# Kernel tuning notes

Measured on AMD Instinct MI355X. Metric: run time of the kernel, lower is better.

## Reference

```python
import jax, jax.numpy as jnp
import numpy as np

B, T, S, H = 8, 256, 256, 512

def setup_inputs() -> dict:
    key = jax.random.key(0)
    k1, k2, k3, k4, k5, k6 = jax.random.split(key, 6)
    query = jax.random.normal(k1, (B, T, H), dtype=jnp.float32)
    encoder_outputs = jax.random.normal(k2, (B, S, H), dtype=jnp.float32)
    # lengths in [1, S] so every row has at least one valid source position
    src_lengths = jax.random.randint(k3, (B,), 1, S + 1, dtype=jnp.int64)
    scale = 1.0 / np.sqrt(H)
    W_h = jax.random.normal(k4, (H, H), dtype=jnp.float32) * scale  # nn.Linear weight (out, in)
    W_s = jax.random.normal(k5, (H, H), dtype=jnp.float32) * scale
    v = jax.random.normal(k6, (H,), dtype=jnp.float32) * scale     # nn.Linear(H,1) weight squeezed
    return {"query": query, "encoder_outputs": encoder_outputs,
            "src_lengths": src_lengths, "W_h": W_h, "W_s": W_s, "v": v}

def reference(query, encoder_outputs, src_lengths, W_h, W_s, v):
    # Linear without bias: y = x @ W^T
    enc_f = jnp.einsum('bsh,oh->bso', encoder_outputs, W_h)   # (B,S,H)
    qry_f = jnp.einsum('bth,oh->bto', query, W_s)             # (B,T,H)
    # additive score: v^T tanh(enc_f + qry_f), broadcast over (T,S)
    scores = jnp.einsum('btsh,h->bts',
                        jnp.tanh(enc_f[:, None, :, :] + qry_f[:, :, None, :]), v)  # (B,T,S)
    mask = jnp.arange(S)[None, :] >= src_lengths[:, None]      # (B,S) True = pad
    scores = jnp.where(mask[:, None, :], -jnp.inf, scores)
    attn_weights = jax.nn.softmax(scores, axis=-1)             # (B,T,S)
    attn_out = jnp.einsum('bts,bsh->bth', attn_weights, encoder_outputs)
    return attn_out
```

## Files before the change

kernel.cpp:

```cpp
#include <hip/hip_runtime.h>
#include <hip/hip_cooperative_groups.h>
#include <cstddef>
#include <math.h>

namespace cg = cooperative_groups;

#define BD 8
#define TD 256
#define SD 256
#define HD 512
#define K2F 2.885390081777927f

#define EXP2(x) __builtin_amdgcn_exp2f(x)
#define RCP(x)  __builtin_amdgcn_rcpf(x)

typedef __attribute__((ext_vector_type(8))) _Float16 half8;
typedef __attribute__((ext_vector_type(4))) _Float16 half4;
typedef __attribute__((ext_vector_type(4))) float float4v;

__device__ __forceinline__ float exp2_sat(float x) {
    return EXP2(fminf(fmaxf(x, -80.0f), 80.0f));
}

#define LSTR 40

__global__ __launch_bounds__(512) void fused_kernel(
    const float* __restrict__ enc,
    const float* __restrict__ qry,
    const float* __restrict__ Wh,
    const float* __restrict__ Ws,
    const float* __restrict__ v,
    const int*   __restrict__ lens,
    float* __restrict__ encT,
    float* __restrict__ qryf,
    float* __restrict__ out)
{
    __shared__ float smem[7168];

    const int bid = blockIdx.x;
    const int tid = threadIdx.x;
    const int l   = tid & 63;
    const int w   = tid >> 6;
    const int rf  = l & 15;
    const int q   = l >> 4;

    {
        _Float16* LA = (_Float16*)smem;
        _Float16* LB = (_Float16*)(smem + 1280);

        const int x  = bid & 7;
        const int k  = bid >> 3;
        const bool isq = k >= 32;
        const int kk = k & 31;
        const int my = (isq ? 32 : 0) + x * 4 + (kk & 3);
        const int n0 = (kk >> 2) * 64;
        const int m0 = my * 64;

        const int srow = tid >> 3;
        const int scol = (tid & 7) * 4;
        const float* Abase = isq
            ? qry + (size_t)(m0 - 2048 + srow) * HD + scol
            : enc + (size_t)(m0 + srow) * HD + scol;
        const float* Bbase = (isq ? Ws : Wh) + (size_t)(n0 + srow) * HD + scol;

        const int mi = (w & 3) * 16;
        const int ni = (w >> 2) * 32;

        float4v acc[2] = {{0,0,0,0},{0,0,0,0}};

        float4 a0 = *(const float4*)(Abase);
        float4 b0 = *(const float4*)(Bbase);

        for (int ks = 0; ks < 16; ++ks) {
            if (ks) __syncthreads();
            {
                half4 ha, hb;
                ha[0]=(_Float16)a0.x; ha[1]=(_Float16)a0.y; ha[2]=(_Float16)a0.z; ha[3]=(_Float16)a0.w;
                hb[0]=(_Float16)b0.x; hb[1]=(_Float16)b0.y; hb[2]=(_Float16)b0.z; hb[3]=(_Float16)b0.w;
                *(half4*)&LA[srow * LSTR + scol] = ha;
                *(half4*)&LB[srow * LSTR + scol] = hb;
            }
            __syncthreads();
            if (ks + 1 < 16) {
                const int ko = (ks + 1) * 32;
                a0 = *(const float4*)(Abase + ko);
                b0 = *(const float4*)(Bbase + ko);
            }
            half8 ah = *(const half8*)&LA[(mi + rf) * LSTR + q * 8];
            #pragma unroll
            for (int j = 0; j < 2; ++j) {
                half8 bh = *(const half8*)&LB[(ni + j * 16 + rf) * LSTR + q * 8];
                acc[j] = __builtin_amdgcn_mfma_f32_16x16x32_f16(ah, bh, acc[j], 0, 0, 0);
            }
        }

        if (!isq) {
            const int b  = m0 >> 8;
            const int sb = (m0 & 255) + mi + q * 4;
            float* base = encT + (size_t)b * HD * SD;
            #pragma unroll
            for (int j = 0; j < 2; ++j) {
                float4 o = make_float4(exp2_sat(acc[j][0]*K2F), exp2_sat(acc[j][1]*K2F),
                                       exp2_sat(acc[j][2]*K2F), exp2_sat(acc[j][3]*K2F));
                *(float4*)(base + (size_t)(n0 + ni + j * 16 + rf) * SD + sb) = o;
            }
        } else {
            const int mrow = (m0 - 2048) + mi + q * 4;
            #pragma unroll
            for (int j = 0; j < 2; ++j)
                #pragma unroll
                for (int r = 0; r < 4; ++r)
                    qryf[(size_t)(mrow + r) * HD + n0 + ni + j * 16 + rf] =
                        exp2_sat(acc[j][r] * K2F);
        }
    }

    cg::this_grid().sync();

    {
        float* qls = smem;
        float* pls = smem + 2048;
        float* wls = smem + 6144;

        const int b  = bid & 7;
        const int t0 = (bid >> 3) * 4;

        {
            const float* qf = qryf + ((size_t)b * TD + t0) * HD;
            float4 qv;
            qv.x = qf[0 * HD + tid]; qv.y = qf[1 * HD + tid];
            qv.z = qf[2 * HD + tid]; qv.w = qf[3 * HD + tid];
            *(float4*)&qls[tid * 4] = qv;
        }
        __syncthreads();

        float a[4][4];
        #pragma unroll
        for (int t = 0; t < 4; ++t)
            #pragma unroll
            for (int c = 0; c < 4; ++c) a[t][c] = 0.0f;
        {
            const float* ep = encT + (size_t)b * HD * SD + (size_t)(w * 64) * SD + l * 4;
            const int jbase = w * 64;
            #pragma unroll 4
            for (int jj = 0; jj < 64; ++jj) {
                float4 e = *(const float4*)(ep + (size_t)jj * SD);
                float4 q4 = *(const float4*)&qls[(jbase + jj) * 4];
                float vj = v[jbase + jj];
                float ev[4] = {e.x, e.y, e.z, e.w};
                float qv[4] = {q4.x, q4.y, q4.z, q4.w};
                #pragma unroll
                for (int t = 0; t < 4; ++t)
                    #pragma unroll
                    for (int c = 0; c < 4; ++c) {
                        float p = fmaf(ev[c], qv[t], 1.0f);
                        a[t][c] = fmaf(vj, RCP(p), a[t][c]);
                    }
            }
        }
        if (w < 4) {
            #pragma unroll
            for (int t = 0; t < 4; ++t)
                *(float4*)&pls[(w * 4 + t) * 256 + l * 4] =
                    make_float4(a[t][0], a[t][1], a[t][2], a[t][3]);
        }
        __syncthreads();
        if (w >= 4) {
            #pragma unroll
            for (int t = 0; t < 4; ++t) {
                float4 c4 = *(const float4*)&pls[((w - 4) * 4 + t) * 256 + l * 4];
                c4.x += a[t][0]; c4.y += a[t][1]; c4.z += a[t][2]; c4.w += a[t][3];
                *(float4*)&pls[((w - 4) * 4 + t) * 256 + l * 4] = c4;
            }
        }
        __syncthreads();

        if (w < 4) {
            const int t = w;
            float p[4] = {0, 0, 0, 0};
            #pragma unroll
            for (int g = 0; g < 4; ++g) {
                float4 pp = *(const float4*)&pls[(g * 4 + t) * 256 + l * 4];
                p[0] += pp.x; p[1] += pp.y; p[2] += pp.z; p[3] += pp.w;
            }
            const int len = lens[b];
            const int s0 = l * 4;
            float sc[4];
            #pragma unroll
            for (int c = 0; c < 4; ++c)
                sc[c] = (s0 + c < len) ? -2.0f * p[c] : -INFINITY;
            float mx = fmaxf(fmaxf(sc[0], sc[1]), fmaxf(sc[2], sc[3]));
            #pragma unroll
            for (int off = 32; off; off >>= 1) mx = fmaxf(mx, __shfl_xor(mx, off));
            float ex[4]; float sum = 0.0f;
            #pragma unroll
            for (int c = 0; c < 4; ++c) { ex[c] = __expf(sc[c] - mx); sum += ex[c]; }
            #pragma unroll
            for (int off = 32; off; off >>= 1) sum += __shfl_xor(sum, off);
            const float inv = RCP(sum);
            *(float4*)&wls[t * SD + s0] = make_float4(ex[0]*inv, ex[1]*inv, ex[2]*inv, ex[3]*inv);
        }
        __syncthreads();

        const int sg = tid >> 7;
        const int h4 = (tid & 127) * 4;
        float* avred = pls;
        float4 o[4] = {{0,0,0,0},{0,0,0,0},{0,0,0,0},{0,0,0,0}};
        {
            const float* eb = enc + (size_t)b * SD * HD + h4;
            #pragma unroll 2
            for (int ss = 0; ss < 64; ++ss) {
                const int s = sg * 64 + ss;
                float4 evv = *(const float4*)(eb + (size_t)s * HD);
                float wt[4];
                #pragma unroll
                for (int t = 0; t < 4; ++t) wt[t] = wls[t * SD + s];
                #pragma unroll
                for (int t = 0; t < 4; ++t) {
                    o[t].x = fmaf(wt[t], evv.x, o[t].x);
                    o[t].y = fmaf(wt[t], evv.y, o[t].y);
                    o[t].z = fmaf(wt[t], evv.z, o[t].z);
                    o[t].w = fmaf(wt[t], evv.w, o[t].w);
                }
            }
        }
        if (sg < 2) {
            #pragma unroll
            for (int t = 0; t < 4; ++t)
                *(float4*)&avred[(size_t)(sg * 4 + t) * 512 + h4] = o[t];
        }
        __syncthreads();
        if (sg >= 2) {
            #pragma unroll
            for (int t = 0; t < 4; ++t) {
                float4 c4 = *(const float4*)&avred[(size_t)((sg - 2) * 4 + t) * 512 + h4];
                c4.x += o[t].x; c4.y += o[t].y; c4.z += o[t].z; c4.w += o[t].w;
                *(float4*)&avred[(size_t)((sg - 2) * 4 + t) * 512 + h4] = c4;
            }
        }
        __syncthreads();

        {
            const int t  = tid >> 7;
            const int hh = (tid & 127) * 4;
            float4 x0 = *(const float4*)&avred[(size_t)(0 * 4 + t) * 512 + hh];
            float4 x1 = *(const float4*)&avred[(size_t)(1 * 4 + t) * 512 + hh];
            float4 r = make_float4(x0.x + x1.x, x0.y + x1.y, x0.z + x1.z, x0.w + x1.w);
            *(float4*)(out + ((size_t)b * TD + t0 + t) * HD + hh) = r;
        }
    }
}

__global__ __launch_bounds__(256) void proj_fb(
    const float* __restrict__ enc, const float* __restrict__ qry,
    const float* __restrict__ Wh,  const float* __restrict__ Ws,
    float* __restrict__ encT, float* __restrict__ qryf)
{
    __shared__ _Float16 LA[64 * LSTR], LB[64 * LSTR];

    const int tid = threadIdx.x;
    const int l = tid & 63, w = tid >> 6;
    const int rf = l & 15, q = l >> 4;
    const int my = blockIdx.y;
    const bool isq = my >= 32;
    const int m0 = my * 64;
    const int n0 = blockIdx.x * 64;

    const int srow = tid >> 2;
    const int scol = (tid & 3) * 8;
    const float* Abase = isq
        ? qry + (size_t)(m0 - 2048 + srow) * HD + scol
        : enc + (size_t)(m0 + srow) * HD + scol;
    const float* Bbase = (isq ? Ws : Wh) + (size_t)(n0 + srow) * HD + scol;

    const int mi = (w & 1) * 32, ni = (w >> 1) * 32;
    float4v acc[2][2] = {{{0,0,0,0},{0,0,0,0}},{{0,0,0,0},{0,0,0,0}}};

    float4 a0 = *(const float4*)(Abase);
    float4 a1 = *(const float4*)(Abase + 4);
    float4 b0 = *(const float4*)(Bbase);
    float4 b1 = *(const float4*)(Bbase + 4);

    for (int ks = 0; ks < 16; ++ks) {
        if (ks) __syncthreads();
        {
            float af[8] = {a0.x,a0.y,a0.z,a0.w,a1.x,a1.y,a1.z,a1.w};
            float bf[8] = {b0.x,b0.y,b0.z,b0.w,b1.x,b1.y,b1.z,b1.w};
            half8 ha, hb;
            #pragma unroll
            for (int i = 0; i < 8; ++i) { ha[i] = (_Float16)af[i]; hb[i] = (_Float16)bf[i]; }
            *(half8*)&LA[srow * LSTR + scol] = ha;
            *(half8*)&LB[srow * LSTR + scol] = hb;
        }
        __syncthreads();
        if (ks + 1 < 16) {
            const int ko = (ks + 1) * 32;
            a0 = *(const float4*)(Abase + ko);
            a1 = *(const float4*)(Abase + ko + 4);
            b0 = *(const float4*)(Bbase + ko);
            b1 = *(const float4*)(Bbase + ko + 4);
        }
        half8 ah[2], bh[2];
        #pragma unroll
        for (int i = 0; i < 2; ++i) {
            ah[i] = *(const half8*)&LA[(mi + i * 16 + rf) * LSTR + q * 8];
            bh[i] = *(const half8*)&LB[(ni + i * 16 + rf) * LSTR + q * 8];
        }
        #pragma unroll
        for (int i = 0; i < 2; ++i)
            #pragma unroll
            for (int j = 0; j < 2; ++j)
                acc[i][j] = __builtin_amdgcn_mfma_f32_16x16x32_f16(ah[i], bh[j], acc[i][j], 0, 0, 0);
    }

    if (!isq) {
        const int b  = m0 >> 8;
        const int sb = (m0 & 255) + mi + q * 4;
        float* base = encT + (size_t)b * HD * SD;
        #pragma unroll
        for (int i = 0; i < 2; ++i)
            #pragma unroll
            for (int j = 0; j < 2; ++j) {
                float4 o = make_float4(exp2_sat(acc[i][j][0]*K2F), exp2_sat(acc[i][j][1]*K2F),
                                       exp2_sat(acc[i][j][2]*K2F), exp2_sat(acc[i][j][3]*K2F));
                *(float4*)(base + (size_t)(n0 + ni + j * 16 + rf) * SD + sb + i * 16) = o;
            }
    } else {
        const int mrow = (m0 - 2048) + mi + q * 4;
        #pragma unroll
        for (int i = 0; i < 2; ++i)
            #pragma unroll
            for (int j = 0; j < 2; ++j)
                #pragma unroll
                for (int r = 0; r < 4; ++r)
                    qryf[(size_t)(mrow + i * 16 + r) * HD + n0 + ni + j * 16 + rf] =
                        exp2_sat(acc[i][j][r] * K2F);
    }
}

__global__ __launch_bounds__(512) void attn_fb(
    const float* __restrict__ enc, const float* __restrict__ encT,
    const float* __restrict__ qryf, const float* __restrict__ v,
    const int* __restrict__ lens, float* __restrict__ out)
{
    __shared__ float qls[HD * 4];
    __shared__ float pls[8 * 4 * 256];
    __shared__ float wls[4 * SD];

    const int blk = blockIdx.x;
    const int b   = blk >> 6;
    const int t0  = (blk & 63) * 4;
    const int tid = threadIdx.x;
    const int w   = tid >> 6;
    const int l   = tid & 63;

    {
        const float* qf = qryf + ((size_t)b * TD + t0) * HD;
        float4 qv;
        qv.x = qf[0 * HD + tid]; qv.y = qf[1 * HD + tid];
        qv.z = qf[2 * HD + tid]; qv.w = qf[3 * HD + tid];
        *(float4*)&qls[tid * 4] = qv;
    }
    __syncthreads();

    float a[4][4];
    #pragma unroll
    for (int t = 0; t < 4; ++t)
        #pragma unroll
        for (int c = 0; c < 4; ++c) a[t][c] = 0.0f;
    {
        const float* ep = encT + (size_t)b * HD * SD + (size_t)(w * 64) * SD + l * 4;
        const int jbase = w * 64;
        #pragma unroll 4
        for (int jj = 0; jj < 64; ++jj) {
            float4 e = *(const float4*)(ep + (size_t)jj * SD);
            float4 q4 = *(const float4*)&qls[(jbase + jj) * 4];
            float vj = v[jbase + jj];
            float ev[4] = {e.x, e.y, e.z, e.w};
            float qv[4] = {q4.x, q4.y, q4.z, q4.w};
            #pragma unroll
            for (int t = 0; t < 4; ++t)
                #pragma unroll
                for (int c = 0; c < 4; ++c) {
                    float p = fmaf(ev[c], qv[t], 1.0f);
                    a[t][c] = fmaf(vj, RCP(p), a[t][c]);
                }
        }
    }
    #pragma unroll
    for (int t = 0; t < 4; ++t)
        *(float4*)&pls[(w * 4 + t) * 256 + l * 4] = make_float4(a[t][0], a[t][1], a[t][2], a[t][3]);
    __syncthreads();

    if (w < 4) {
        const int t = w;
        float p[4] = {0, 0, 0, 0};
        #pragma unroll
        for (int g = 0; g < 8; ++g) {
            float4 pp = *(const float4*)&pls[(g * 4 + t) * 256 + l * 4];
            p[0] += pp.x; p[1] += pp.y; p[2] += pp.z; p[3] += pp.w;
        }
        const int len = lens[b];
        const int s0 = l * 4;
        float sc[4];
        #pragma unroll
        for (int c = 0; c < 4; ++c)
            sc[c] = (s0 + c < len) ? -2.0f * p[c] : -INFINITY;
        float mx = fmaxf(fmaxf(sc[0], sc[1]), fmaxf(sc[2], sc[3]));
        #pragma unroll
        for (int off = 32; off; off >>= 1) mx = fmaxf(mx, __shfl_xor(mx, off));
        float ex[4]; float sum = 0.0f;
        #pragma unroll
        for (int c = 0; c < 4; ++c) { ex[c] = __expf(sc[c] - mx); sum += ex[c]; }
        #pragma unroll
        for (int off = 32; off; off >>= 1) sum += __shfl_xor(sum, off);
        const float inv = RCP(sum);
        *(float4*)&wls[t * SD + s0] = make_float4(ex[0]*inv, ex[1]*inv, ex[2]*inv, ex[3]*inv);
    }
    __syncthreads();

    const int g  = tid >> 7;
    const int h4 = (tid & 127) * 4;
    float* avred = pls;
    {
        const float* eb = enc + (size_t)b * SD * HD + h4;
        float4 o[4] = {{0,0,0,0},{0,0,0,0},{0,0,0,0},{0,0,0,0}};
        #pragma unroll 2
        for (int ss = 0; ss < 64; ++ss) {
            const int s = g * 64 + ss;
            float4 evv = *(const float4*)(eb + (size_t)s * HD);
            float wt[4];
            #pragma unroll
            for (int t = 0; t < 4; ++t) wt[t] = wls[t * SD + s];
            #pragma unroll
            for (int t = 0; t < 4; ++t) {
                o[t].x = fmaf(wt[t], evv.x, o[t].x);
                o[t].y = fmaf(wt[t], evv.y, o[t].y);
                o[t].z = fmaf(wt[t], evv.z, o[t].z);
                o[t].w = fmaf(wt[t], evv.w, o[t].w);
            }
        }
        #pragma unroll
        for (int t = 0; t < 4; ++t)
            *(float4*)&avred[(size_t)(g * 4 + t) * 512 + h4] = o[t];
    }
    __syncthreads();
    {
        const int t  = tid >> 7;
        const int hh = (tid & 127) * 4;
        float4 r = {0, 0, 0, 0};
        #pragma unroll
        for (int gg = 0; gg < 4; ++gg) {
            float4 x = *(const float4*)&avred[(size_t)(gg * 4 + t) * 512 + hh];
            r.x += x.x; r.y += x.y; r.z += x.z; r.w += x.w;
        }
        *(float4*)(out + ((size_t)b * TD + t0 + t) * HD + hh) = r;
    }
}

extern "C" void kernel_launch(void* const* d_in, const int* in_sizes, int n_in,
                              void* d_out, int out_size, void* d_ws, size_t ws_size,
                              hipStream_t stream) {
    const float* query = (const float*)d_in[0];
    const float* enc   = (const float*)d_in[1];
    const int*   lens  = (const int*)d_in[2];
    const float* W_h   = (const float*)d_in[3];
    const float* W_s   = (const float*)d_in[4];
    const float* v     = (const float*)d_in[5];
    float* out = (float*)d_out;

    char* ws = (char*)d_ws;
    float* encT = (float*)(ws);
    float* qryf = (float*)(ws + ((size_t)4 << 20));

    int nb = 0;
    hipError_t oerr = hipOccupancyMaxActiveBlocksPerMultiprocessor(
        &nb, (const void*)fused_kernel, 512, 0);
    bool coop_ok = (oerr == hipSuccess) && (nb * 256 >= 512);

    if (coop_ok) {
        void* args[] = {
            (void*)&enc, (void*)&query, (void*)&W_h, (void*)&W_s,
            (void*)&v, (void*)&lens, (void*)&encT, (void*)&qryf, (void*)&out
        };
        hipError_t lerr = hipLaunchCooperativeKernel((const void*)fused_kernel,
                                                     dim3(512), dim3(512), args, 0, stream);
        if (lerr == hipSuccess) return;
    }

    dim3 pgrid(HD / 64, 64);
    proj_fb<<<pgrid, 256, 0, stream>>>(enc, query, W_h, W_s, encT, qryf);
    attn_fb<<<BD * (TD / 4), 512, 0, stream>>>(enc, encT, qryf, v, lens, out);
}
```

Measured before the change: 121.0 us.

## Split attention phase across 1024 cooperative blocks with two timesteps each

```diff
diff --git a/kernel.cpp b/kernel.cpp
--- a/kernel.cpp
+++ b/kernel.cpp
@@ -24,231 +24,254 @@
 
 #define LSTR 40
 
-__global__ __launch_bounds__(512) void fused_kernel(
-    const float* __restrict__ enc,
-    const float* __restrict__ qry,
-    const float* __restrict__ Wh,
-    const float* __restrict__ Ws,
-    const float* __restrict__ v,
-    const int*   __restrict__ lens,
-    float* __restrict__ encT,
-    float* __restrict__ qryf,
-    float* __restrict__ out)
+__device__ __forceinline__ void phaseA(
+    int bid, int tid, float* smem,
+    const float* __restrict__ enc, const float* __restrict__ qry,
+    const float* __restrict__ Wh,  const float* __restrict__ Ws,
+    float* __restrict__ encT, float* __restrict__ qryf)
+{
+    const int l  = tid & 63;
+    const int w  = tid >> 6;
+    const int rf = l & 15;
+    const int q  = l >> 4;
+
+    _Float16* LA = (_Float16*)smem;
+    _Float16* LB = (_Float16*)(smem + 1280);
+
+    const int x  = bid & 7;
+    const int k  = bid >> 3;
+    const bool isq = k >= 32;
+    const int kk = k & 31;
+    const int my = (isq ? 32 : 0) + x * 4 + (kk & 3);
+    const int n0 = (kk >> 2) * 64;
+    const int m0 = my * 64;
+
+    const int srow = tid >> 3;
+    const int scol = (tid & 7) * 4;
+    const float* Abase = isq
+        ? qry + (size_t)(m0 - 2048 + srow) * HD + scol
+        : enc + (size_t)(m0 + srow) * HD + scol;
+    const float* Bbase = (isq ? Ws : Wh) + (size_t)(n0 + srow) * HD + scol;
+
+    const int mi = (w & 3) * 16;
+    const int ni = (w >> 2) * 32;
+
+    float4v acc[2] = {{0,0,0,0},{0,0,0,0}};
+
+    float4 a0 = *(const float4*)(Abase);
+    float4 b0 = *(const float4*)(Bbase);
+
+    for (int ks = 0; ks < 16; ++ks) {
+        if (ks) __syncthreads();
+        {
+            half4 ha, hb;
+            ha[0]=(_Float16)a0.x; ha[1]=(_Float16)a0.y; ha[2]=(_Float16)a0.z; ha[3]=(_Float16)a0.w;
+            hb[0]=(_Float16)b0.x; hb[1]=(_Float16)b0.y; hb[2]=(_Float16)b0.z; hb[3]=(_Float16)b0.w;
+            *(half4*)&LA[srow * LSTR + scol] = ha;
+            *(half4*)&LB[srow * LSTR + scol] = hb;
+        }
+        __syncthreads();
+        if (ks + 1 < 16) {
+            const int ko = (ks + 1) * 32;
+            a0 = *(const float4*)(Abase + ko);
+            b0 = *(const float4*)(Bbase + ko);
+        }
+        half8 ah = *(const half8*)&LA[(mi + rf) * LSTR + q * 8];
+        #pragma unroll
+        for (int j = 0; j < 2; ++j) {
+            half8 bh = *(const half8*)&LB[(ni + j * 16 + rf) * LSTR + q * 8];
+            acc[j] = __builtin_amdgcn_mfma_f32_16x16x32_f16(ah, bh, acc[j], 0, 0, 0);
+        }
+    }
+
+    if (!isq) {
+        const int b  = m0 >> 8;
+        const int sb = (m0 & 255) + mi + q * 4;
+        float* base = encT + (size_t)b * HD * SD;
+        #pragma unroll
+        for (int j = 0; j < 2; ++j) {
+            float4 o = make_float4(exp2_sat(acc[j][0]*K2F), exp2_sat(acc[j][1]*K2F),
+                                   exp2_sat(acc[j][2]*K2F), exp2_sat(acc[j][3]*K2F));
+            *(float4*)(base + (size_t)(n0 + ni + j * 16 + rf) * SD + sb) = o;
+        }
+    } else {
+        const int mrow = (m0 - 2048) + mi + q * 4;
+        #pragma unroll
+        for (int j = 0; j < 2; ++j)
+            #pragma unroll
+            for (int r = 0; r < 4; ++r)
+                qryf[(size_t)(mrow + r) * HD + n0 + ni + j * 16 + rf] =
+                    exp2_sat(acc[j][r] * K2F);
+    }
+}
+
+template<int TT>
+__device__ __forceinline__ void phaseB(
+    int b, int t0, int tid, float* smem,
+    const float* __restrict__ enc, const float* __restrict__ encT,
+    const float* __restrict__ qryf, const float* __restrict__ v,
+    const int* __restrict__ lens, float* __restrict__ out)
+{
+    const int l = tid & 63;
+    const int w = tid >> 6;
+
+    float* qls = smem;
+    float* pls = smem + 512 * TT;
+    float* wls = smem + 1536 * TT;
+
+    {
+        const float* qf = qryf + ((size_t)b * TD + t0) * HD;
+        #pragma unroll
+        for (int t = 0; t < TT; ++t) qls[tid * TT + t] = qf[t * HD + tid];
+    }
+    __syncthreads();
+
+    float a[TT][4];
+    #pragma unroll
+    for (int t = 0; t < TT; ++t)
+        #pragma unroll
+        for (int c = 0; c < 4; ++c) a[t][c] = 0.0f;
+    {
+        const float* ep = encT + (size_t)b * HD * SD + (size_t)(w * 64) * SD + l * 4;
+        const int jbase = w * 64;
+        #pragma unroll 4
+        for (int jj = 0; jj < 64; ++jj) {
+            float4 e = *(const float4*)(ep + (size_t)jj * SD);
+            float vj = v[jbase + jj];
+            float qv[TT];
+            #pragma unroll
+            for (int t = 0; t < TT; ++t) qv[t] = qls[(jbase + jj) * TT + t];
+            float ev[4] = {e.x, e.y, e.z, e.w};
+            #pragma unroll
+            for (int t = 0; t < TT; ++t)
+                #pragma unroll
+                for (int c = 0; c < 4; ++c) {
+                    float p = fmaf(ev[c], qv[t], 1.0f);
+                    a[t][c] = fmaf(vj, RCP(p), a[t][c]);
+                }
+        }
+    }
+    if (w < 4) {
+        #pragma unroll
+        for (int t = 0; t < TT; ++t)
+            *(float4*)&pls[(w * TT + t) * 256 + l * 4] =
+                make_float4(a[t][0], a[t][1], a[t][2], a[t][3]);
+    }
+    __syncthreads();
+    if (w >= 4) {
+        #pragma unroll
+        for (int t = 0; t < TT; ++t) {
+            float4 c4 = *(const float4*)&pls[((w - 4) * TT + t) * 256 + l * 4];
+            c4.x += a[t][0]; c4.y += a[t][1]; c4.z += a[t][2]; c4.w += a[t][3];
+            *(float4*)&pls[((w - 4) * TT + t) * 256 + l * 4] = c4;
+        }
+    }
+    __syncthreads();
+
+    if (w < TT) {
+        const int t = w;
+        float p[4] = {0, 0, 0, 0};
+        #pragma unroll
+        for (int g = 0; g < 4; ++g) {
+            float4 pp = *(const float4*)&pls[(g * TT + t) * 256 + l * 4];
+            p[0] += pp.x; p[1] += pp.y; p[2] += pp.z; p[3] += pp.w;
+        }
+        const int len = lens[b];
+        const int s0 = l * 4;
+        float sc[4];
+        #pragma unroll
+        for (int c = 0; c < 4; ++c)
+            sc[c] = (s0 + c < len) ? -2.0f * p[c] : -INFINITY;
+        float mx = fmaxf(fmaxf(sc[0], sc[1]), fmaxf(sc[2], sc[3]));
+        #pragma unroll
+        for (int off = 32; off; off >>= 1) mx = fmaxf(mx, __shfl_xor(mx, off));
+        float ex[4]; float sum = 0.0f;
+        #pragma unroll
+        for (int c = 0; c < 4; ++c) { ex[c] = __expf(sc[c] - mx); sum += ex[c]; }
+        #pragma unroll
+        for (int off = 32; off; off >>= 1) sum += __shfl_xor(sum, off);
+        const float inv = RCP(sum);
+        *(float4*)&wls[t * SD + s0] = make_float4(ex[0]*inv, ex[1]*inv, ex[2]*inv, ex[3]*inv);
+    }
+    __syncthreads();
+
+    const int sg = tid >> 7;
+    const int h4 = (tid & 127) * 4;
+    float* avred = pls;
+    float4 o[TT];
+    #pragma unroll
+    for (int t = 0; t < TT; ++t) o[t] = make_float4(0.f, 0.f, 0.f, 0.f);
+    {
+        const float* eb = enc + (size_t)b * SD * HD + h4;
+        #pragma unroll 2
+        for (int ss = 0; ss < 64; ++ss) {
+            const int s = sg * 64 + ss;
+            float4 evv = *(const float4*)(eb + (size_t)s * HD);
+            float wt[TT];
+            #pragma unroll
+            for (int t = 0; t < TT; ++t) wt[t] = wls[t * SD + s];
+            #pragma unroll
+            for (int t = 0; t < TT; ++t) {
+                o[t].x = fmaf(wt[t], evv.x, o[t].x);
+                o[t].y = fmaf(wt[t], evv.y, o[t].y);
+                o[t].z = fmaf(wt[t], evv.z, o[t].z);
+                o[t].w = fmaf(wt[t], evv.w, o[t].w);
+            }
+        }
+    }
+    if (sg < 2) {
+        #pragma unroll
+        for (int t = 0; t < TT; ++t)
+            *(float4*)&avred[(size_t)(sg * TT + t) * 512 + h4] = o[t];
+    }
+    __syncthreads();
+    if (sg >= 2) {
+        #pragma unroll
+        for (int t = 0; t < TT; ++t) {
+            float4 c4 = *(const float4*)&avred[(size_t)((sg - 2) * TT + t) * 512 + h4];
+            c4.x += o[t].x; c4.y += o[t].y; c4.z += o[t].z; c4.w += o[t].w;
+            *(float4*)&avred[(size_t)((sg - 2) * TT + t) * 512 + h4] = c4;
+        }
+    }
+    __syncthreads();
+
+    if (tid < TT * 128) {
+        const int t  = tid >> 7;
+        const int hh = (tid & 127) * 4;
+        float4 x0 = *(const float4*)&avred[(size_t)(0 * TT + t) * 512 + hh];
+        float4 x1 = *(const float4*)&avred[(size_t)(1 * TT + t) * 512 + hh];
+        float4 r = make_float4(x0.x + x1.x, x0.y + x1.y, x0.z + x1.z, x0.w + x1.w);
+        *(float4*)(out + ((size_t)b * TD + t0 + t) * HD + hh) = r;
+    }
+}
+
+__global__ __launch_bounds__(512) void fused1024(
+    const float* __restrict__ enc, const float* __restrict__ qry,
+    const float* __restrict__ Wh,  const float* __restrict__ Ws,
+    const float* __restrict__ v,   const int* __restrict__ lens,
+    float* __restrict__ encT, float* __restrict__ qryf, float* __restrict__ out)
+{
+    __shared__ float smem[3584];
+    const int bid = blockIdx.x;
+    if (bid < 512)
+        phaseA(bid, threadIdx.x, smem, enc, qry, Wh, Ws, encT, qryf);
+    cg::this_grid().sync();
+    phaseB<2>(bid & 7, (bid >> 3) * 2, threadIdx.x, smem,
+              enc, encT, qryf, v, lens, out);
+}
+
+__global__ __launch_bounds__(512) void fused512(
+    const float* __restrict__ enc, const float* __restrict__ qry,
+    const float* __restrict__ Wh,  const float* __restrict__ Ws,
+    const float* __restrict__ v,   const int* __restrict__ lens,
+    float* __restrict__ encT, float* __restrict__ qryf, float* __restrict__ out)
 {
     __shared__ float smem[7168];
-
     const int bid = blockIdx.x;
-    const int tid = threadIdx.x;
-    const int l   = tid & 63;
-    const int w   = tid >> 6;
-    const int rf  = l & 15;
-    const int q   = l >> 4;
-
-    {
-        _Float16* LA = (_Float16*)smem;
-        _Float16* LB = (_Float16*)(smem + 1280);
-
-        const int x  = bid & 7;
-        const int k  = bid >> 3;
-        const bool isq = k >= 32;
-        const int kk = k & 31;
-        const int my = (isq ? 32 : 0) + x * 4 + (kk & 3);
-        const int n0 = (kk >> 2) * 64;
-        const int m0 = my * 64;
-
-        const int srow = tid >> 3;
-        const int scol = (tid & 7) * 4;
-        const float* Abase = isq
-            ? qry + (size_t)(m0 - 2048 + srow) * HD + scol
-            : enc + (size_t)(m0 + srow) * HD + scol;
-        const float* Bbase = (isq ? Ws : Wh) + (size_t)(n0 + srow) * HD + scol;
-
-        const int mi = (w & 3) * 16;
-        const int ni = (w >> 2) * 32;
-
-        float4v acc[2] = {{0,0,0,0},{0,0,0,0}};
-
-        float4 a0 = *(const float4*)(Abase);
-        float4 b0 = *(const float4*)(Bbase);
-
-        for (int ks = 0; ks < 16; ++ks) {
-            if (ks) __syncthreads();
-            {
-                half4 ha, hb;
-                ha[0]=(_Float16)a0.x; ha[1]=(_Float16)a0.y; ha[2]=(_Float16)a0.z; ha[3]=(_Float16)a0.w;
-                hb[0]=(_Float16)b0.x; hb[1]=(_Float16)b0.y; hb[2]=(_Float16)b0.z; hb[3]=(_Float16)b0.w;
-                *(half4*)&LA[srow * LSTR + scol] = ha;
-                *(half4*)&LB[srow * LSTR + scol] = hb;
-            }
-            __syncthreads();
-            if (ks + 1 < 16) {
-                const int ko = (ks + 1) * 32;
-                a0 = *(const float4*)(Abase + ko);
-                b0 = *(const float4*)(Bbase + ko);
-            }
-            half8 ah = *(const half8*)&LA[(mi + rf) * LSTR + q * 8];
-            #pragma unroll
-            for (int j = 0; j < 2; ++j) {
-                half8 bh = *(const half8*)&LB[(ni + j * 16 + rf) * LSTR + q * 8];
-                acc[j] = __builtin_amdgcn_mfma_f32_16x16x32_f16(ah, bh, acc[j], 0, 0, 0);
-            }
-        }
-
-        if (!isq) {
-            const int b  = m0 >> 8;
-            const int sb = (m0 & 255) + mi + q * 4;
-            float* base = encT + (size_t)b * HD * SD;
-            #pragma unroll
-            for (int j = 0; j < 2; ++j) {
-                float4 o = make_float4(exp2_sat(acc[j][0]*K2F), exp2_sat(acc[j][1]*K2F),
-                                       exp2_sat(acc[j][2]*K2F), exp2_sat(acc[j][3]*K2F));
-                *(float4*)(base + (size_t)(n0 + ni + j * 16 + rf) * SD + sb) = o;
-            }
-        } else {
-            const int mrow = (m0 - 2048) + mi + q * 4;
-            #pragma unroll
-            for (int j = 0; j < 2; ++j)
-                #pragma unroll
-                for (int r = 0; r < 4; ++r)
-                    qryf[(size_t)(mrow + r) * HD + n0 + ni + j * 16 + rf] =
-                        exp2_sat(acc[j][r] * K2F);
-        }
-    }
-
+    phaseA(bid, threadIdx.x, smem, enc, qry, Wh, Ws, encT, qryf);
     cg::this_grid().sync();
-
-    {
-        float* qls = smem;
-        float* pls = smem + 2048;
-        float* wls = smem + 6144;
-
-        const int b  = bid & 7;
-        const int t0 = (bid >> 3) * 4;
-
-        {
-            const float* qf = qryf + ((size_t)b * TD + t0) * HD;
-            float4 qv;
-            qv.x = qf[0 * HD + tid]; qv.y = qf[1 * HD + tid];
-            qv.z = qf[2 * HD + tid]; qv.w = qf[3 * HD + tid];
-            *(float4*)&qls[tid * 4] = qv;
-        }
-        __syncthreads();
-
-        float a[4][4];
-        #pragma unroll
-        for (int t = 0; t < 4; ++t)
-            #pragma unroll
-            for (int c = 0; c < 4; ++c) a[t][c] = 0.0f;
-        {
-            const float* ep = encT + (size_t)b * HD * SD + (size_t)(w * 64) * SD + l * 4;
-            const int jbase = w * 64;
-            #pragma unroll 4
-            for (int jj = 0; jj < 64; ++jj) {
-                float4 e = *(const float4*)(ep + (size_t)jj * SD);
-                float4 q4 = *(const float4*)&qls[(jbase + jj) * 4];
-                float vj = v[jbase + jj];
-                float ev[4] = {e.x, e.y, e.z, e.w};
-                float qv[4] = {q4.x, q4.y, q4.z, q4.w};
-                #pragma unroll
-                for (int t = 0; t < 4; ++t)
-                    #pragma unroll
-                    for (int c = 0; c < 4; ++c) {
-                        float p = fmaf(ev[c], qv[t], 1.0f);
-                        a[t][c] = fmaf(vj, RCP(p), a[t][c]);
-                    }
-            }
-        }
-        if (w < 4) {
-            #pragma unroll
-            for (int t = 0; t < 4; ++t)
-                *(float4*)&pls[(w * 4 + t) * 256 + l * 4] =
-                    make_float4(a[t][0], a[t][1], a[t][2], a[t][3]);
-        }
-        __syncthreads();
-        if (w >= 4) {
-            #pragma unroll
-            for (int t = 0; t < 4; ++t) {
-                float4 c4 = *(const float4*)&pls[((w - 4) * 4 + t) * 256 + l * 4];
-                c4.x += a[t][0]; c4.y += a[t][1]; c4.z += a[t][2]; c4.w += a[t][3];
-                *(float4*)&pls[((w - 4) * 4 + t) * 256 + l * 4] = c4;
-            }
-        }
-        __syncthreads();
-
-        if (w < 4) {
-            const int t = w;
-            float p[4] = {0, 0, 0, 0};
-            #pragma unroll
-            for (int g = 0; g < 4; ++g) {
-                float4 pp = *(const float4*)&pls[(g * 4 + t) * 256 + l * 4];
-                p[0] += pp.x; p[1] += pp.y; p[2] += pp.z; p[3] += pp.w;
-            }
-            const int len = lens[b];
-            const int s0 = l * 4;
-            float sc[4];
-            #pragma unroll
-            for (int c = 0; c < 4; ++c)
-                sc[c] = (s0 + c < len) ? -2.0f * p[c] : -INFINITY;
-            float mx = fmaxf(fmaxf(sc[0], sc[1]), fmaxf(sc[2], sc[3]));
-            #pragma unroll
-            for (int off = 32; off; off >>= 1) mx = fmaxf(mx, __shfl_xor(mx, off));
-            float ex[4]; float sum = 0.0f;
-            #pragma unroll
-            for (int c = 0; c < 4; ++c) { ex[c] = __expf(sc[c] - mx); sum += ex[c]; }
-            #pragma unroll
-            for (int off = 32; off; off >>= 1) sum += __shfl_xor(sum, off);
-            const float inv = RCP(sum);
-            *(float4*)&wls[t * SD + s0] = make_float4(ex[0]*inv, ex[1]*inv, ex[2]*inv, ex[3]*inv);
-        }
-        __syncthreads();
-
-        const int sg = tid >> 7;
-        const int h4 = (tid & 127) * 4;
-        float* avred = pls;
-        float4 o[4] = {{0,0,0,0},{0,0,0,0},{0,0,0,0},{0,0,0,0}};
-        {
-            const float* eb = enc + (size_t)b * SD * HD + h4;
-            #pragma unroll 2
-            for (int ss = 0; ss < 64; ++ss) {
-                const int s = sg * 64 + ss;
-                float4 evv = *(const float4*)(eb + (size_t)s * HD);
-                float wt[4];
-                #pragma unroll
-                for (int t = 0; t < 4; ++t) wt[t] = wls[t * SD + s];
-                #pragma unroll
-                for (int t = 0; t < 4; ++t) {
-                    o[t].x = fmaf(wt[t], evv.x, o[t].x);
-                    o[t].y = fmaf(wt[t], evv.y, o[t].y);
-                    o[t].z = fmaf(wt[t], evv.z, o[t].z);
-                    o[t].w = fmaf(wt[t], evv.w, o[t].w);
-                }
-            }
-        }
-        if (sg < 2) {
-            #pragma unroll
-            for (int t = 0; t < 4; ++t)
-                *(float4*)&avred[(size_t)(sg * 4 + t) * 512 + h4] = o[t];
-        }
-        __syncthreads();
-        if (sg >= 2) {
-            #pragma unroll
-            for (int t = 0; t < 4; ++t) {
-                float4 c4 = *(const float4*)&avred[(size_t)((sg - 2) * 4 + t) * 512 + h4];
-                c4.x += o[t].x; c4.y += o[t].y; c4.z += o[t].z; c4.w += o[t].w;
-                *(float4*)&avred[(size_t)((sg - 2) * 4 + t) * 512 + h4] = c4;
-            }
-        }
-        __syncthreads();
-
-        {
-            const int t  = tid >> 7;
-            const int hh = (tid & 127) * 4;
-            float4 x0 = *(const float4*)&avred[(size_t)(0 * 4 + t) * 512 + hh];
-            float4 x1 = *(const float4*)&avred[(size_t)(1 * 4 + t) * 512 + hh];
-            float4 r = make_float4(x0.x + x1.x, x0.y + x1.y, x0.z + x1.z, x0.w + x1.w);
-            *(float4*)(out + ((size_t)b * TD + t0 + t) * HD + hh) = r;
-        }
-    }
+    phaseB<4>(bid & 7, (bid >> 3) * 4, threadIdx.x, smem,
+              enc, encT, qryf, v, lens, out);
 }
 
 __global__ __launch_bounds__(256) void proj_fb(
@@ -473,17 +496,25 @@
     float* encT = (float*)(ws);
     float* qryf = (float*)(ws + ((size_t)4 << 20));
 
+    void* args[] = {
+        (void*)&enc, (void*)&query, (void*)&W_h, (void*)&W_s,
+        (void*)&v, (void*)&lens, (void*)&encT, (void*)&qryf, (void*)&out
+    };
+
     int nb = 0;
     hipError_t oerr = hipOccupancyMaxActiveBlocksPerMultiprocessor(
-        &nb, (const void*)fused_kernel, 512, 0);
-    bool coop_ok = (oerr == hipSuccess) && (nb * 256 >= 512);
-
-    if (coop_ok) {
-        void* args[] = {
-            (void*)&enc, (void*)&query, (void*)&W_h, (void*)&W_s,
-            (void*)&v, (void*)&lens, (void*)&encT, (void*)&qryf, (void*)&out
-        };
-        hipError_t lerr = hipLaunchCooperativeKernel((const void*)fused_kernel,
+        &nb, (const void*)fused1024, 512, 0);
+    if (oerr == hipSuccess && nb >= 4) {
+        hipError_t lerr = hipLaunchCooperativeKernel((const void*)fused1024,
+                                                     dim3(1024), dim3(512), args, 0, stream);
+        if (lerr == hipSuccess) return;
+    }
+
+    nb = 0;
+    oerr = hipOccupancyMaxActiveBlocksPerMultiprocessor(
+        &nb, (const void*)fused512, 512, 0);
+    if (oerr == hipSuccess && nb >= 2) {
+        hipError_t lerr = hipLaunchCooperativeKernel((const void*)fused512,
                                                      dim3(512), dim3(512), args, 0, stream);
         if (lerr == hipSuccess) return;
     }
```

Result: no change. 120.8 us (-0.1%).

## Replace cooperative fused kernel with two 1024-thread kernels and 8-row attention tiles

Applied to the files above, without the earlier changes.

```diff
diff --git a/kernel.cpp b/kernel.cpp
--- a/kernel.cpp
+++ b/kernel.cpp
@@ -1,9 +1,6 @@
 #include <hip/hip_runtime.h>
-#include <hip/hip_cooperative_groups.h>
 #include <cstddef>
 #include <math.h>
-
-namespace cg = cooperative_groups;
 
 #define BD 8
 #define TD 256
@@ -24,362 +21,121 @@
 
 #define LSTR 40
 
-__global__ __launch_bounds__(512) void fused_kernel(
-    const float* __restrict__ enc,
-    const float* __restrict__ qry,
-    const float* __restrict__ Wh,
-    const float* __restrict__ Ws,
-    const float* __restrict__ v,
-    const int*   __restrict__ lens,
-    float* __restrict__ encT,
-    float* __restrict__ qryf,
-    float* __restrict__ out)
-{
-    __shared__ float smem[7168];
-
-    const int bid = blockIdx.x;
-    const int tid = threadIdx.x;
-    const int l   = tid & 63;
-    const int w   = tid >> 6;
-    const int rf  = l & 15;
-    const int q   = l >> 4;
-
-    {
-        _Float16* LA = (_Float16*)smem;
-        _Float16* LB = (_Float16*)(smem + 1280);
-
-        const int x  = bid & 7;
-        const int k  = bid >> 3;
-        const bool isq = k >= 32;
-        const int kk = k & 31;
-        const int my = (isq ? 32 : 0) + x * 4 + (kk & 3);
-        const int n0 = (kk >> 2) * 64;
-        const int m0 = my * 64;
-
-        const int srow = tid >> 3;
-        const int scol = (tid & 7) * 4;
-        const float* Abase = isq
-            ? qry + (size_t)(m0 - 2048 + srow) * HD + scol
-            : enc + (size_t)(m0 + srow) * HD + scol;
-        const float* Bbase = (isq ? Ws : Wh) + (size_t)(n0 + srow) * HD + scol;
-
-        const int mi = (w & 3) * 16;
-        const int ni = (w >> 2) * 32;
-
-        float4v acc[2] = {{0,0,0,0},{0,0,0,0}};
-
-        float4 a0 = *(const float4*)(Abase);
-        float4 b0 = *(const float4*)(Bbase);
-
-        for (int ks = 0; ks < 16; ++ks) {
-            if (ks) __syncthreads();
-            {
-                half4 ha, hb;
-                ha[0]=(_Float16)a0.x; ha[1]=(_Float16)a0.y; ha[2]=(_Float16)a0.z; ha[3]=(_Float16)a0.w;
-                hb[0]=(_Float16)b0.x; hb[1]=(_Float16)b0.y; hb[2]=(_Float16)b0.z; hb[3]=(_Float16)b0.w;
-                *(half4*)&LA[srow * LSTR + scol] = ha;
-                *(half4*)&LB[srow * LSTR + scol] = hb;
-            }
-            __syncthreads();
-            if (ks + 1 < 16) {
-                const int ko = (ks + 1) * 32;
-                a0 = *(const float4*)(Abase + ko);
-                b0 = *(const float4*)(Bbase + ko);
-            }
-            half8 ah = *(const half8*)&LA[(mi + rf) * LSTR + q * 8];
-            #pragma unroll
-            for (int j = 0; j < 2; ++j) {
-                half8 bh = *(const half8*)&LB[(ni + j * 16 + rf) * LSTR + q * 8];
-                acc[j] = __builtin_amdgcn_mfma_f32_16x16x32_f16(ah, bh, acc[j], 0, 0, 0);
-            }
-        }
-
-        if (!isq) {
-            const int b  = m0 >> 8;
-            const int sb = (m0 & 255) + mi + q * 4;
-            float* base = encT + (size_t)b * HD * SD;
-            #pragma unroll
-            for (int j = 0; j < 2; ++j) {
-                float4 o = make_float4(exp2_sat(acc[j][0]*K2F), exp2_sat(acc[j][1]*K2F),
-                                       exp2_sat(acc[j][2]*K2F), exp2_sat(acc[j][3]*K2F));
-                *(float4*)(base + (size_t)(n0 + ni + j * 16 + rf) * SD + sb) = o;
-            }
-        } else {
-            const int mrow = (m0 - 2048) + mi + q * 4;
-            #pragma unroll
-            for (int j = 0; j < 2; ++j)
-                #pragma unroll
-                for (int r = 0; r < 4; ++r)
-                    qryf[(size_t)(mrow + r) * HD + n0 + ni + j * 16 + rf] =
-                        exp2_sat(acc[j][r] * K2F);
-        }
-    }
-
-    cg::this_grid().sync();
-
-    {
-        float* qls = smem;
-        float* pls = smem + 2048;
-        float* wls = smem + 6144;
-
-        const int b  = bid & 7;
-        const int t0 = (bid >> 3) * 4;
-
-        {
-            const float* qf = qryf + ((size_t)b * TD + t0) * HD;
-            float4 qv;
-            qv.x = qf[0 * HD + tid]; qv.y = qf[1 * HD + tid];
-            qv.z = qf[2 * HD + tid]; qv.w = qf[3 * HD + tid];
-            *(float4*)&qls[tid * 4] = qv;
-        }
-        __syncthreads();
-
-        float a[4][4];
-        #pragma unroll
-        for (int t = 0; t < 4; ++t)
-            #pragma unroll
-            for (int c = 0; c < 4; ++c) a[t][c] = 0.0f;
-        {
-            const float* ep = encT + (size_t)b * HD * SD + (size_t)(w * 64) * SD + l * 4;
-            const int jbase = w * 64;
-            #pragma unroll 4
-            for (int jj = 0; jj < 64; ++jj) {
-                float4 e = *(const float4*)(ep + (size_t)jj * SD);
-                float4 q4 = *(const float4*)&qls[(jbase + jj) * 4];
-                float vj = v[jbase + jj];
-                float ev[4] = {e.x, e.y, e.z, e.w};
-                float qv[4] = {q4.x, q4.y, q4.z, q4.w};
-                #pragma unroll
-                for (int t = 0; t < 4; ++t)
-                    #pragma unroll
-                    for (int c = 0; c < 4; ++c) {
-                        float p = fmaf(ev[c], qv[t], 1.0f);
-                        a[t][c] = fmaf(vj, RCP(p), a[t][c]);
-                    }
-            }
-        }
-        if (w < 4) {
-            #pragma unroll
-            for (int t = 0; t < 4; ++t)
-                *(float4*)&pls[(w * 4 + t) * 256 + l * 4] =
-                    make_float4(a[t][0], a[t][1], a[t][2], a[t][3]);
-        }
-        __syncthreads();
-        if (w >= 4) {
-            #pragma unroll
-            for (int t = 0; t < 4; ++t) {
-                float4 c4 = *(const float4*)&pls[((w - 4) * 4 + t) * 256 + l * 4];
-                c4.x += a[t][0]; c4.y += a[t][1]; c4.z += a[t][2]; c4.w += a[t][3];
-                *(float4*)&pls[((w - 4) * 4 + t) * 256 + l * 4] = c4;
-            }
-        }
-        __syncthreads();
-
-        if (w < 4) {
-            const int t = w;
-            float p[4] = {0, 0, 0, 0};
-            #pragma unroll
-            for (int g = 0; g < 4; ++g) {
-                float4 pp = *(const float4*)&pls[(g * 4 + t) * 256 + l * 4];
-                p[0] += pp.x; p[1] += pp.y; p[2] += pp.z; p[3] += pp.w;
-            }
-            const int len = lens[b];
-            const int s0 = l * 4;
-            float sc[4];
-            #pragma unroll
-            for (int c = 0; c < 4; ++c)
-                sc[c] = (s0 + c < len) ? -2.0f * p[c] : -INFINITY;
-            float mx = fmaxf(fmaxf(sc[0], sc[1]), fmaxf(sc[2], sc[3]));
-            #pragma unroll
-            for (int off = 32; off; off >>= 1) mx = fmaxf(mx, __shfl_xor(mx, off));
-            float ex[4]; float sum = 0.0f;
-            #pragma unroll
-            for (int c = 0; c < 4; ++c) { ex[c] = __expf(sc[c] - mx); sum += ex[c]; }
-            #pragma unroll
-            for (int off = 32; off; off >>= 1) sum += __shfl_xor(sum, off);
-            const float inv = RCP(sum);
-            *(float4*)&wls[t * SD + s0] = make_float4(ex[0]*inv, ex[1]*inv, ex[2]*inv, ex[3]*inv);
-        }
-        __syncthreads();
-
-        const int sg = tid >> 7;
-        const int h4 = (tid & 127) * 4;
-        float* avred = pls;
-        float4 o[4] = {{0,0,0,0},{0,0,0,0},{0,0,0,0},{0,0,0,0}};
-        {
-            const float* eb = enc + (size_t)b * SD * HD + h4;
-            #pragma unroll 2
-            for (int ss = 0; ss < 64; ++ss) {
-                const int s = sg * 64 + ss;
-                float4 evv = *(const float4*)(eb + (size_t)s * HD);
-                float wt[4];
-                #pragma unroll
-                for (int t = 0; t < 4; ++t) wt[t] = wls[t * SD + s];
-                #pragma unroll
-                for (int t = 0; t < 4; ++t) {
-                    o[t].x = fmaf(wt[t], evv.x, o[t].x);
-                    o[t].y = fmaf(wt[t], evv.y, o[t].y);
-                    o[t].z = fmaf(wt[t], evv.z, o[t].z);
-                    o[t].w = fmaf(wt[t], evv.w, o[t].w);
-                }
-            }
-        }
-        if (sg < 2) {
-            #pragma unroll
-            for (int t = 0; t < 4; ++t)
-                *(float4*)&avred[(size_t)(sg * 4 + t) * 512 + h4] = o[t];
-        }
-        __syncthreads();
-        if (sg >= 2) {
-            #pragma unroll
-            for (int t = 0; t < 4; ++t) {
-                float4 c4 = *(const float4*)&avred[(size_t)((sg - 2) * 4 + t) * 512 + h4];
-                c4.x += o[t].x; c4.y += o[t].y; c4.z += o[t].z; c4.w += o[t].w;
-                *(float4*)&avred[(size_t)((sg - 2) * 4 + t) * 512 + h4] = c4;
-            }
-        }
-        __syncthreads();
-
-        {
-            const int t  = tid >> 7;
-            const int hh = (tid & 127) * 4;
-            float4 x0 = *(const float4*)&avred[(size_t)(0 * 4 + t) * 512 + hh];
-            float4 x1 = *(const float4*)&avred[(size_t)(1 * 4 + t) * 512 + hh];
-            float4 r = make_float4(x0.x + x1.x, x0.y + x1.y, x0.z + x1.z, x0.w + x1.w);
-            *(float4*)(out + ((size_t)b * TD + t0 + t) * HD + hh) = r;
-        }
-    }
-}
-
-__global__ __launch_bounds__(256) void proj_fb(
+__global__ __launch_bounds__(1024) void projK(
     const float* __restrict__ enc, const float* __restrict__ qry,
     const float* __restrict__ Wh,  const float* __restrict__ Ws,
     float* __restrict__ encT, float* __restrict__ qryf)
 {
-    __shared__ _Float16 LA[64 * LSTR], LB[64 * LSTR];
-
+    __shared__ float smem[2560];
+
+    const int bid = blockIdx.x;
     const int tid = threadIdx.x;
-    const int l = tid & 63, w = tid >> 6;
-    const int rf = l & 15, q = l >> 4;
-    const int my = blockIdx.y;
-    const bool isq = my >= 32;
+    const int l  = tid & 63;
+    const int w  = tid >> 6;
+    const int rf = l & 15;
+    const int q  = l >> 4;
+
+    _Float16* LA = (_Float16*)smem;
+    _Float16* LB = (_Float16*)(smem + 1280);
+
+    const int x  = bid & 7;
+    const int k  = bid >> 3;
+    const bool isq = k >= 32;
+    const int kk = k & 31;
+    const int my = (isq ? 32 : 0) + x * 4 + (kk & 3);
+    const int n0 = (kk >> 2) * 64;
     const int m0 = my * 64;
-    const int n0 = blockIdx.x * 64;
-
-    const int srow = tid >> 2;
-    const int scol = (tid & 3) * 8;
-    const float* Abase = isq
-        ? qry + (size_t)(m0 - 2048 + srow) * HD + scol
-        : enc + (size_t)(m0 + srow) * HD + scol;
-    const float* Bbase = (isq ? Ws : Wh) + (size_t)(n0 + srow) * HD + scol;
-
-    const int mi = (w & 1) * 32, ni = (w >> 1) * 32;
-    float4v acc[2][2] = {{{0,0,0,0},{0,0,0,0}},{{0,0,0,0},{0,0,0,0}}};
-
-    float4 a0 = *(const float4*)(Abase);
-    float4 a1 = *(const float4*)(Abase + 4);
-    float4 b0 = *(const float4*)(Bbase);
-    float4 b1 = *(const float4*)(Bbase + 4);
+
+    const bool stagesA = (tid < 512);
+    const int srow = (tid >> 3) & 63;
+    const int scol = (tid & 7) * 4;
+    const float* Sbase = stagesA
+        ? (isq ? qry + (size_t)(m0 - 2048 + srow) * HD
+               : enc + (size_t)(m0 + srow) * HD) + scol
+        : (isq ? Ws : Wh) + (size_t)(n0 + srow) * HD + scol;
+    _Float16* Ldst = (stagesA ? LA : LB) + srow * LSTR + scol;
+
+    const int mi = (w & 3) * 16;
+    const int ni = (w >> 2) * 16;
+
+    float4v acc = {0, 0, 0, 0};
+
+    float4 a0 = *(const float4*)(Sbase);
 
     for (int ks = 0; ks < 16; ++ks) {
         if (ks) __syncthreads();
         {
-            float af[8] = {a0.x,a0.y,a0.z,a0.w,a1.x,a1.y,a1.z,a1.w};
-            float bf[8] = {b0.x,b0.y,b0.z,b0.w,b1.x,b1.y,b1.z,b1.w};
-            half8 ha, hb;
-            #pragma unroll
-            for (int i = 0; i < 8; ++i) { ha[i] = (_Float16)af[i]; hb[i] = (_Float16)bf[i]; }
-            *(half8*)&LA[srow * LSTR + scol] = ha;
-            *(half8*)&LB[srow * LSTR + scol] = hb;
+            half4 ha;
+            ha[0]=(_Float16)a0.x; ha[1]=(_Float16)a0.y; ha[2]=(_Float16)a0.z; ha[3]=(_Float16)a0.w;
+            *(half4*)Ldst = ha;
         }
         __syncthreads();
-        if (ks + 1 < 16) {
-            const int ko = (ks + 1) * 32;
-            a0 = *(const float4*)(Abase + ko);
-            a1 = *(const float4*)(Abase + ko + 4);
-            b0 = *(const float4*)(Bbase + ko);
-            b1 = *(const float4*)(Bbase + ko + 4);
-        }
-        half8 ah[2], bh[2];
-        #pragma unroll
-        for (int i = 0; i < 2; ++i) {
-            ah[i] = *(const half8*)&LA[(mi + i * 16 + rf) * LSTR + q * 8];
-            bh[i] = *(const half8*)&LB[(ni + i * 16 + rf) * LSTR + q * 8];
-        }
-        #pragma unroll
-        for (int i = 0; i < 2; ++i)
-            #pragma unroll
-            for (int j = 0; j < 2; ++j)
-                acc[i][j] = __builtin_amdgcn_mfma_f32_16x16x32_f16(ah[i], bh[j], acc[i][j], 0, 0, 0);
+        if (ks + 1 < 16) a0 = *(const float4*)(Sbase + (ks + 1) * 32);
+        half8 ah = *(const half8*)&LA[(mi + rf) * LSTR + q * 8];
+        half8 bh = *(const half8*)&LB[(ni + rf) * LSTR + q * 8];
+        acc = __builtin_amdgcn_mfma_f32_16x16x32_f16(ah, bh, acc, 0, 0, 0);
     }
 
     if (!isq) {
         const int b  = m0 >> 8;
         const int sb = (m0 & 255) + mi + q * 4;
         float* base = encT + (size_t)b * HD * SD;
-        #pragma unroll
-        for (int i = 0; i < 2; ++i)
-            #pragma unroll
-            for (int j = 0; j < 2; ++j) {
-                float4 o = make_float4(exp2_sat(acc[i][j][0]*K2F), exp2_sat(acc[i][j][1]*K2F),
-                                       exp2_sat(acc[i][j][2]*K2F), exp2_sat(acc[i][j][3]*K2F));
-                *(float4*)(base + (size_t)(n0 + ni + j * 16 + rf) * SD + sb + i * 16) = o;
-            }
+        float4 o = make_float4(exp2_sat(acc[0]*K2F), exp2_sat(acc[1]*K2F),
+                               exp2_sat(acc[2]*K2F), exp2_sat(acc[3]*K2F));
+        *(float4*)(base + (size_t)(n0 + ni + rf) * SD + sb) = o;
     } else {
         const int mrow = (m0 - 2048) + mi + q * 4;
         #pragma unroll
-        for (int i = 0; i < 2; ++i)
-            #pragma unroll
-            for (int j = 0; j < 2; ++j)
-                #pragma unroll
-                for (int r = 0; r < 4; ++r)
-                    qryf[(size_t)(mrow + i * 16 + r) * HD + n0 + ni + j * 16 + rf] =
-                        exp2_sat(acc[i][j][r] * K2F);
-    }
-}
-
-__global__ __launch_bounds__(512) void attn_fb(
+        for (int r = 0; r < 4; ++r)
+            qryf[(size_t)(mrow + r) * HD + n0 + ni + rf] = exp2_sat(acc[r] * K2F);
+    }
+}
+
+__global__ __launch_bounds__(1024) void attnK(
     const float* __restrict__ enc, const float* __restrict__ encT,
     const float* __restrict__ qryf, const float* __restrict__ v,
     const int* __restrict__ lens, float* __restrict__ out)
 {
-    __shared__ float qls[HD * 4];
-    __shared__ float pls[8 * 4 * 256];
-    __shared__ float wls[4 * SD];
-
-    const int blk = blockIdx.x;
-    const int b   = blk >> 6;
-    const int t0  = (blk & 63) * 4;
+    __shared__ float smem[14336];
+
+    const int bid = blockIdx.x;
     const int tid = threadIdx.x;
-    const int w   = tid >> 6;
-    const int l   = tid & 63;
+    const int b   = bid & 7;
+    const int t0  = (bid >> 3) * 8;
+    const int l = tid & 63;
+    const int w = tid >> 6;
+
+    float* qls = smem;
+    float* pls = smem + 4096;
+    float* wls = smem + 12288;
 
     {
         const float* qf = qryf + ((size_t)b * TD + t0) * HD;
-        float4 qv;
-        qv.x = qf[0 * HD + tid]; qv.y = qf[1 * HD + tid];
-        qv.z = qf[2 * HD + tid]; qv.w = qf[3 * HD + tid];
-        *(float4*)&qls[tid * 4] = qv;
-    }
-    __syncthreads();
-
-    float a[4][4];
+        const int j = tid & 511;
+        #pragma unroll
+        for (int t = (tid >> 9); t < 8; t += 2)
+            qls[t * 512 + j] = qf[t * HD + j];
+    }
+    __syncthreads();
+
+    float a[8][4];
     #pragma unroll
-    for (int t = 0; t < 4; ++t)
+    for (int t = 0; t < 8; ++t)
         #pragma unroll
         for (int c = 0; c < 4; ++c) a[t][c] = 0.0f;
     {
-        const float* ep = encT + (size_t)b * HD * SD + (size_t)(w * 64) * SD + l * 4;
-        const int jbase = w * 64;
+        const int jbase = w * 32;
+        const float* ep = encT + (size_t)b * HD * SD + (size_t)jbase * SD + l * 4;
         #pragma unroll 4
-        for (int jj = 0; jj < 64; ++jj) {
+        for (int jj = 0; jj < 32; ++jj) {
             float4 e = *(const float4*)(ep + (size_t)jj * SD);
-            float4 q4 = *(const float4*)&qls[(jbase + jj) * 4];
             float vj = v[jbase + jj];
+            float qv[8];
+            #pragma unroll
+            for (int t = 0; t < 8; ++t) qv[t] = qls[t * 512 + jbase + jj];
             float ev[4] = {e.x, e.y, e.z, e.w};
-            float qv[4] = {q4.x, q4.y, q4.z, q4.w};
-            #pragma unroll
-            for (int t = 0; t < 4; ++t)
+            #pragma unroll
+            for (int t = 0; t < 8; ++t)
                 #pragma unroll
                 for (int c = 0; c < 4; ++c) {
                     float p = fmaf(ev[c], qv[t], 1.0f);
@@ -387,17 +143,47 @@
                 }
         }
     }
-    #pragma unroll
-    for (int t = 0; t < 4; ++t)
-        *(float4*)&pls[(w * 4 + t) * 256 + l * 4] = make_float4(a[t][0], a[t][1], a[t][2], a[t][3]);
-    __syncthreads();
-
     if (w < 4) {
+        #pragma unroll
+        for (int t = 0; t < 8; ++t)
+            *(float4*)&pls[(w * 8 + t) * 256 + l * 4] =
+                make_float4(a[t][0], a[t][1], a[t][2], a[t][3]);
+    }
+    __syncthreads();
+    if (w >= 4 && w < 8) {
+        #pragma unroll
+        for (int t = 0; t < 8; ++t) {
+            float4 c4 = *(const float4*)&pls[((w - 4) * 8 + t) * 256 + l * 4];
+            c4.x += a[t][0]; c4.y += a[t][1]; c4.z += a[t][2]; c4.w += a[t][3];
+            *(float4*)&pls[((w - 4) * 8 + t) * 256 + l * 4] = c4;
+        }
+    }
+    __syncthreads();
+    if (w >= 8 && w < 12) {
+        #pragma unroll
+        for (int t = 0; t < 8; ++t) {
+            float4 c4 = *(const float4*)&pls[((w - 8) * 8 + t) * 256 + l * 4];
+            c4.x += a[t][0]; c4.y += a[t][1]; c4.z += a[t][2]; c4.w += a[t][3];
+            *(float4*)&pls[((w - 8) * 8 + t) * 256 + l * 4] = c4;
+        }
+    }
+    __syncthreads();
+    if (w >= 12) {
+        #pragma unroll
+        for (int t = 0; t < 8; ++t) {
+            float4 c4 = *(const float4*)&pls[((w - 12) * 8 + t) * 256 + l * 4];
+            c4.x += a[t][0]; c4.y += a[t][1]; c4.z += a[t][2]; c4.w += a[t][3];
+            *(float4*)&pls[((w - 12) * 8 + t) * 256 + l * 4] = c4;
+        }
+    }
+    __syncthreads();
+
+    if (w < 8) {
         const int t = w;
         float p[4] = {0, 0, 0, 0};
         #pragma unroll
-        for (int g = 0; g < 8; ++g) {
-            float4 pp = *(const float4*)&pls[(g * 4 + t) * 256 + l * 4];
+        for (int g = 0; g < 4; ++g) {
+            float4 pp = *(const float4*)&pls[(g * 8 + t) * 256 + l * 4];
             p[0] += pp.x; p[1] += pp.y; p[2] += pp.z; p[3] += pp.w;
         }
         const int len = lens[b];
@@ -419,41 +205,70 @@
     }
     __syncthreads();
 
-    const int g  = tid >> 7;
+    const int sg = tid >> 7;
     const int h4 = (tid & 127) * 4;
     float* avred = pls;
+    float4 o[8];
+    #pragma unroll
+    for (int t = 0; t < 8; ++t) o[t] = make_float4(0.f, 0.f, 0.f, 0.f);
     {
         const float* eb = enc + (size_t)b * SD * HD + h4;
-        float4 o[4] = {{0,0,0,0},{0,0,0,0},{0,0,0,0},{0,0,0,0}};
         #pragma unroll 2
-        for (int ss = 0; ss < 64; ++ss) {
-            const int s = g * 64 + ss;
+        for (int ss = 0; ss < 32; ++ss) {
+            const int s = sg * 32 + ss;
             float4 evv = *(const float4*)(eb + (size_t)s * HD);
-            float wt[4];
-            #pragma unroll
-            for (int t = 0; t < 4; ++t) wt[t] = wls[t * SD + s];
-            #pragma unroll
-            for (int t = 0; t < 4; ++t) {
+            float wt[8];
+            #pragma unroll
+            for (int t = 0; t < 8; ++t) wt[t] = wls[t * SD + s];
+            #pragma unroll
+            for (int t = 0; t < 8; ++t) {
                 o[t].x = fmaf(wt[t], evv.x, o[t].x);
                 o[t].y = fmaf(wt[t], evv.y, o[t].y);
                 o[t].z = fmaf(wt[t], evv.z, o[t].z);
                 o[t].w = fmaf(wt[t], evv.w, o[t].w);
             }
         }
-        #pragma unroll
-        for (int t = 0; t < 4; ++t)
-            *(float4*)&avred[(size_t)(g * 4 + t) * 512 + h4] = o[t];
-    }
-    __syncthreads();
+    }
+    if (sg < 2) {
+        #pragma unroll
+        for (int t = 0; t < 8; ++t)
+            *(float4*)&avred[(size_t)(sg * 8 + t) * 512 + h4] = o[t];
+    }
+    __syncthreads();
+    if (sg >= 2 && sg < 4) {
+        #pragma unroll
+        for (int t = 0; t < 8; ++t) {
+            float4 c4 = *(const float4*)&avred[(size_t)((sg - 2) * 8 + t) * 512 + h4];
+            c4.x += o[t].x; c4.y += o[t].y; c4.z += o[t].z; c4.w += o[t].w;
+            *(float4*)&avred[(size_t)((sg - 2) * 8 + t) * 512 + h4] = c4;
+        }
+    }
+    __syncthreads();
+    if (sg >= 4 && sg < 6) {
+        #pragma unroll
+        for (int t = 0; t < 8; ++t) {
+            float4 c4 = *(const float4*)&avred[(size_t)((sg - 4) * 8 + t) * 512 + h4];
+            c4.x += o[t].x; c4.y += o[t].y; c4.z += o[t].z; c4.w += o[t].w;
+            *(float4*)&avred[(size_t)((sg - 4) * 8 + t) * 512 + h4] = c4;
+        }
+    }
+    __syncthreads();
+    if (sg >= 6) {
+        #pragma unroll
+        for (int t = 0; t < 8; ++t) {
+            float4 c4 = *(const float4*)&avred[(size_t)((sg - 6) * 8 + t) * 512 + h4];
+            c4.x += o[t].x; c4.y += o[t].y; c4.z += o[t].z; c4.w += o[t].w;
+            *(float4*)&avred[(size_t)((sg - 6) * 8 + t) * 512 + h4] = c4;
+        }
+    }
+    __syncthreads();
+
     {
         const int t  = tid >> 7;
         const int hh = (tid & 127) * 4;
-        float4 r = {0, 0, 0, 0};
-        #pragma unroll
-        for (int gg = 0; gg < 4; ++gg) {
-            float4 x = *(const float4*)&avred[(size_t)(gg * 4 + t) * 512 + hh];
-            r.x += x.x; r.y += x.y; r.z += x.z; r.w += x.w;
-        }
+        float4 x0 = *(const float4*)&avred[(size_t)(0 * 8 + t) * 512 + hh];
+        float4 x1 = *(const float4*)&avred[(size_t)(1 * 8 + t) * 512 + hh];
+        float4 r = make_float4(x0.x + x1.x, x0.y + x1.y, x0.z + x1.z, x0.w + x1.w);
         *(float4*)(out + ((size_t)b * TD + t0 + t) * HD + hh) = r;
     }
 }
@@ -473,22 +288,6 @@
     float* encT = (float*)(ws);
     float* qryf = (float*)(ws + ((size_t)4 << 20));
 
-    int nb = 0;
-    hipError_t oerr = hipOccupancyMaxActiveBlocksPerMultiprocessor(
-        &nb, (const void*)fused_kernel, 512, 0);
-    bool coop_ok = (oerr == hipSuccess) && (nb * 256 >= 512);
-
-    if (coop_ok) {
-        void* args[] = {
-            (void*)&enc, (void*)&query, (void*)&W_h, (void*)&W_s,
-            (void*)&v, (void*)&lens, (void*)&encT, (void*)&qryf, (void*)&out
-        };
-        hipError_t lerr = hipLaunchCooperativeKernel((const void*)fused_kernel,
-                                                     dim3(512), dim3(512), args, 0, stream);
-        if (lerr == hipSuccess) return;
-    }
-
-    dim3 pgrid(HD / 64, 64);
-    proj_fb<<<pgrid, 256, 0, stream>>>(enc, query, W_h, W_s, encT, qryf);
-    attn_fb<<<BD * (TD / 4), 512, 0, stream>>>(enc, encT, qryf, v, lens, out);
-}
+    projK<<<dim3(512), dim3(1024), 0, stream>>>(enc, query, W_h, W_s, encT, qryf);
+    attnK<<<dim3(256), dim3(1024), 0, stream>>>(enc, encT, qryf, v, lens, out);
+}
```

Measured after the change: 119.1 us. No clear change (-1.5%).
